# Performance work log

Hardware: AMD Instinct MI355X
Metric: run time of the kernel (lower is better)

The kernel has to match this reference:

```python
import jax, jax.numpy as jnp
import numpy as np

T, N, E = 3, 100000, 1600000
D_IN, D_H, D_OUT = 64, 64, 1


def _linear_params(key, fan_in, fan_out):
    s = 1.0 / np.sqrt(fan_in)
    k1, k2 = jax.random.split(key)
    W = jax.random.uniform(k1, (fan_in, fan_out), jnp.float32, -s, s)
    b = jax.random.uniform(k2, (fan_out,), jnp.float32, -s, s)
    return W, b


def setup_inputs() -> dict:
    key = jax.random.key(0)
    ks = jax.random.split(key, 9)
    x = jax.random.normal(ks[0], (T, N, D_IN), jnp.float32)
    src = jax.random.randint(ks[1], (T, E), 0, N, jnp.int32)
    dst = jax.random.randint(ks[2], (T, E), 0, N, jnp.int32)
    # xavier-uniform initial GCN weight [D_IN, D_H]
    lim = np.sqrt(6.0 / (D_IN + D_H))
    initial_weight = jax.random.uniform(ks[3], (D_IN, D_H), jnp.float32, -lim, lim)
    Wz, bz = _linear_params(ks[4], D_IN + D_H, D_H)  # update gate
    Wr, br = _linear_params(ks[5], D_IN + D_H, D_H)  # reset gate
    Wh, bh = _linear_params(ks[6], D_IN + D_H, D_H)  # htilda
    Wp, bp = _linear_params(ks[7], D_IN, D_IN)        # pool_proj
    Wo, bo = _linear_params(ks[8], D_H, D_OUT)        # out
    return dict(x=x, src=src, dst=dst, initial_weight=initial_weight,
                Wz=Wz, bz=bz, Wr=Wr, br=br, Wh=Wh, bh=bh,
                Wp=Wp, bp=bp, Wo=Wo, bo=bo)


def reference(x, src, dst, initial_weight, Wz, bz, Wr, br, Wh, bh, Wp, bp, Wo, bo):
    n_nodes = x.shape[1]
    ones_e = jnp.ones((x.shape[2] * 0 + src.shape[1],), jnp.float32)  # [E]

    def step(w, snap):
        xt, st, dt = snap  # [N, D_IN], [E], [E]
        # pooled graph context -> MatGRU weight evolution
        ctx = jnp.mean(xt, axis=0) @ Wp + bp            # [D_IN]
        inp = jnp.broadcast_to(ctx, (D_IN, D_IN))       # inputs.repeat(prev_w.size(0),1)
        xc = jnp.concatenate([inp, w], axis=1)          # [D_IN, D_IN+D_H]
        z = jax.nn.sigmoid(xc @ Wz + bz)
        r = jax.nn.sigmoid(xc @ Wr + br)
        gc = jnp.concatenate([inp, r * w], axis=1)
        h_tilde = jnp.tanh(gc @ Wh + bh)
        w_new = z * w + (1.0 - z) * h_tilde             # [D_IN, D_H]
        # GCN norm: deg = sum of (unit) edge weights per dst, clamp_min 1
        deg = jax.ops.segment_sum(ones_e, dt, num_segments=n_nodes)
        deg = jnp.maximum(deg, 1.0)
        norm = (1.0 / deg)[dt]                          # [E]
        # u_mul_e -> sum aggregation
        agg = jax.ops.segment_sum(xt[st] * norm[:, None], dt, num_segments=n_nodes)
        h = agg @ w_new                                 # [N, D_H]
        out = h @ Wo + bo                               # [N, D_OUT]
        return w_new, out

    w_final, outs = jax.lax.scan(step, initial_weight, (x, src, dst))
    return outs, w_final
```

## Files before the change

kernel.cpp:

```cpp
#include <hip/hip_runtime.h>
#include <math.h>

#define T_STEPS 3
#define N_NODES 100000
#define N_EDGES 1600000
#define N_E4    (N_EDGES / 4)
#define D 64

#define CS_BLOCKS 782

#define BKT_BITS 9
#define BKT_SIZE 512
#define NBKT 196
#define NBKT_PAD 256
#define QSCALE 65536.0f
#define QINV   (1.0f / 65536.0f)

#define SC_EPB 4096
#define SC_I4  1024
#define SC_CHUNKS 391

#define SMV_BLOCKS 782

#define GR_PAD 68

#define PACK_SCALE 1048576.0f
#define PACK_INV   (1.0f / 1048576.0f)


__global__ __launch_bounds__(256) void prep_kernel(const float* __restrict__ x,
                                                   const int* __restrict__ dst,
                                                   float* __restrict__ colsumP,
                                                   unsigned* __restrict__ histChunk) {
    const int t = blockIdx.y;
    const int tid = threadIdx.x;
    __shared__ float red[16][64];
    __shared__ unsigned h[NBKT_PAD];

    if (blockIdx.x < CS_BLOCKS) {
        const int q = tid & 15;
        const int g = tid >> 4;
        const float4* xt = (const float4*)(x + (size_t)t * N_NODES * D);
        const int base = blockIdx.x * 128;
        float sx = 0.f, sy = 0.f, sz = 0.f, sw = 0.f;
#pragma unroll
        for (int it = 0; it < 8; ++it) {
            const int r = base + g + 16 * it;
            if (r < N_NODES) {
                const float4 vv = xt[(size_t)r * 16 + q];
                sx += vv.x; sy += vv.y; sz += vv.z; sw += vv.w;
            }
        }
        red[g][q * 4 + 0] = sx;
        red[g][q * 4 + 1] = sy;
        red[g][q * 4 + 2] = sz;
        red[g][q * 4 + 3] = sw;
        __syncthreads();
        if (tid < 64) {
            float s = 0.f;
#pragma unroll
            for (int gg = 0; gg < 16; ++gg) s += red[gg][tid];
            colsumP[((size_t)t * CS_BLOCKS + blockIdx.x) * 64 + tid] = s;
        }
    } else {
        const int c = blockIdx.x - CS_BLOCKS;
        h[tid] = 0;
        __syncthreads();
        const int4* dp = (const int4*)(dst + (size_t)t * N_EDGES);
#pragma unroll
        for (int it = 0; it < 4; ++it) {
            const int i4 = c * SC_I4 + it * 256 + tid;
            if (i4 < N_E4) {
                const int4 d = dp[i4];
                atomicAdd(&h[d.x >> BKT_BITS], 1u);
                atomicAdd(&h[d.y >> BKT_BITS], 1u);
                atomicAdd(&h[d.z >> BKT_BITS], 1u);
                atomicAdd(&h[d.w >> BKT_BITS], 1u);
            }
        }
        __syncthreads();
        histChunk[((size_t)t * SC_CHUNKS + c) * NBKT_PAD + tid] = h[tid];
    }
}

__device__ __forceinline__ float fast_sigmoid(float v) {
    return 1.f / (1.f + __expf(-v));
}
__device__ __forceinline__ float fast_tanh(float v) {
    return 1.f - 2.f / (__expf(2.f * v) + 1.f);
}

__global__ __launch_bounds__(256) void gru_rows_kernel(
    const float* __restrict__ colsumP, const float* __restrict__ iw,
    const float* __restrict__ Wz, const float* __restrict__ bz,
    const float* __restrict__ Wr, const float* __restrict__ br,
    const float* __restrict__ Wh, const float* __restrict__ bh,
    const float* __restrict__ Wp, const float* __restrict__ bp,
    const float* __restrict__ Wo, const unsigned* __restrict__ histChunk,
    unsigned* __restrict__ bstart, unsigned* __restrict__ chunkPref,
    float* __restrict__ v_out, float* __restrict__ w_final) {
    const int tid = threadIdx.x;

    if (blockIdx.x == 16) {
        __shared__ unsigned scn[NBKT_PAD];
        for (int t = 0; t < T_STEPS; ++t) {
            unsigned c = 0;
            for (int k = 0; k < SC_CHUNKS; ++k)
                c += histChunk[((size_t)t * SC_CHUNKS + k) * NBKT_PAD + tid];
            unsigned v = c;
            scn[tid] = v;
            __syncthreads();
            for (int off = 1; off < NBKT_PAD; off <<= 1) {
                const unsigned add = (tid >= off) ? scn[tid - off] : 0u;
                __syncthreads();
                v += add;
                scn[tid] = v;
                __syncthreads();
            }
            bstart[t * NBKT_PAD + tid] = (unsigned)(t * N_EDGES) + (v - c);
            __syncthreads();
        }
        return;
    }
    if (blockIdx.x >= 17) {
        const int idx = blockIdx.x - 17;
        const int t = idx >> 6;
        const int wid = tid >> 6, lane = tid & 63;
        const int b = (idx & 63) * 4 + wid;
        unsigned running = 0;
#pragma unroll
        for (int g = 0; g < 7; ++g) {
            const int c = g * 64 + lane;
            const unsigned val = (c < SC_CHUNKS)
                ? histChunk[((size_t)t * SC_CHUNKS + c) * NBKT_PAD + b] : 0u;
            unsigned incl = val;
#pragma unroll
            for (int off = 1; off < 64; off <<= 1) {
                const unsigned n = __shfl_up(incl, off);
                if (lane >= off) incl += n;
            }
            if (c < SC_CHUNKS)
                chunkPref[((size_t)t * SC_CHUNKS + c) * NBKT_PAD + b] = running + (incl - val);
            running += __shfl(incl, 63);
        }
        return;
    }

    __shared__ float BzT[64 * GR_PAD];
    __shared__ float BrT[64 * GR_PAD];
    __shared__ float BhT[64 * GR_PAD];
    __shared__ float w_lds[4 * 64];
    __shared__ float mean_s[192];
    __shared__ float ctx_s[192];
    __shared__ float czrh_s[576];

#pragma unroll
    for (int it = 0; it < 16; ++it) {
        const int idx = it * 256 + tid;
        const int k = idx >> 6, j = idx & 63;
        BzT[j * GR_PAD + k] = Wz[(64 + k) * 64 + j];
        BrT[j * GR_PAD + k] = Wr[(64 + k) * 64 + j];
        BhT[j * GR_PAD + k] = Wh[(64 + k) * 64 + j];
    }
    if (tid < 192) {
        const int t = tid >> 6, j = tid & 63;
        float s = 0.f;
        for (int bx = 0; bx < CS_BLOCKS; ++bx)
            s += colsumP[((size_t)t * CS_BLOCKS + bx) * 64 + j];
        mean_s[tid] = s * (1.f / (float)N_NODES);
    }
    __syncthreads();
    if (tid < 192) {
        const int t = tid >> 6, j = tid & 63;
        float c = bp[j];
        for (int k = 0; k < 64; ++k)
            c = fmaf(mean_s[t * 64 + k], Wp[k * 64 + j], c);
        ctx_s[tid] = c;
    }
    __syncthreads();
    for (int co = (tid >> 6); co < 9; co += 4) {
        const int t = co / 3, m = co - 3 * t, j = tid & 63;
        const float* W = (m == 0) ? Wz : (m == 1) ? Wr : Wh;
        const float* bb = (m == 0) ? bz : (m == 1) ? br : bh;
        float c = bb[j];
        for (int k = 0; k < 64; ++k)
            c = fmaf(ctx_s[t * 64 + k], W[k * 64 + j], c);
        czrh_s[co * 64 + j] = c;
    }
    __syncthreads();

    const int wid = tid >> 6, lane = tid & 63;
    const int row = blockIdx.x * 4 + wid;
    float* wrow = &w_lds[wid * 64];
    float w = iw[row * 64 + lane];
    const float wo = Wo[lane];

    for (int t = 0; t < T_STEPS; ++t) {
        wrow[lane] = w;
        __syncthreads();
        float az = 0.f, ar = 0.f;
#pragma unroll
        for (int k0 = 0; k0 < 64; k0 += 4) {
            const float4 wv = *(const float4*)&wrow[k0];
            const float4 z4 = *(const float4*)&BzT[lane * GR_PAD + k0];
            const float4 r4 = *(const float4*)&BrT[lane * GR_PAD + k0];
            az = fmaf(wv.x, z4.x, az); az = fmaf(wv.y, z4.y, az);
            az = fmaf(wv.z, z4.z, az); az = fmaf(wv.w, z4.w, az);
            ar = fmaf(wv.x, r4.x, ar); ar = fmaf(wv.y, r4.y, ar);
            ar = fmaf(wv.z, r4.z, ar); ar = fmaf(wv.w, r4.w, ar);
        }
        const float z = fast_sigmoid(az + czrh_s[(t * 3 + 0) * 64 + lane]);
        const float r = fast_sigmoid(ar + czrh_s[(t * 3 + 1) * 64 + lane]);
        const float rw = r * w;
        __syncthreads();
        wrow[lane] = rw;
        __syncthreads();
        float ah = 0.f;
#pragma unroll
        for (int k0 = 0; k0 < 64; k0 += 4) {
            const float4 wv = *(const float4*)&wrow[k0];
            const float4 h4 = *(const float4*)&BhT[lane * GR_PAD + k0];
            ah = fmaf(wv.x, h4.x, ah); ah = fmaf(wv.y, h4.y, ah);
            ah = fmaf(wv.z, h4.z, ah); ah = fmaf(wv.w, h4.w, ah);
        }
        const float h = fast_tanh(ah + czrh_s[(t * 3 + 2) * 64 + lane]);
        w = z * w + (1.f - z) * h;
        float vp = w * wo;
        vp += __shfl_xor(vp, 1);
        vp += __shfl_xor(vp, 2);
        vp += __shfl_xor(vp, 4);
        vp += __shfl_xor(vp, 8);
        vp += __shfl_xor(vp, 16);
        vp += __shfl_xor(vp, 32);
        if (lane == 0) v_out[t * 64 + row] = vp;
        __syncthreads();
    }
    w_final[row * 64 + lane] = w;
}

__global__ __launch_bounds__(512) void scat_smv_kernel(
    const float* __restrict__ x, const float* __restrict__ v,
    const int* __restrict__ src, const int* __restrict__ dst,
    const unsigned* __restrict__ bstart, const unsigned* __restrict__ chunkPref,
    unsigned* __restrict__ recs, float* __restrict__ s) {
    const int t = blockIdx.y;
    const int tid = threadIdx.x;
    __shared__ __align__(16) unsigned char lds_raw[28672];

    if (blockIdx.x >= SC_CHUNKS) {
        float* vs = (float*)lds_raw;
        if (tid < 64) vs[tid] = v[t * 64 + tid];
        __syncthreads();
        const int row = (blockIdx.x - SC_CHUNKS) * 128 + (tid >> 2);
        const int l4 = tid & 3;
        if (row < N_NODES) {
            const float4* xr = (const float4*)(x + ((size_t)t * N_NODES + row) * D);
            float acc = 0.f;
#pragma unroll
            for (int i = 0; i < 4; ++i) {
                const int c = i * 4 + l4;
                const float4 xv = xr[c];
                acc += xv.x * vs[c * 4 + 0] + xv.y * vs[c * 4 + 1] +
                       xv.z * vs[c * 4 + 2] + xv.w * vs[c * 4 + 3];
            }
            acc += __shfl_xor(acc, 1);
            acc += __shfl_xor(acc, 2);
            if (l4 == 0) s[(size_t)t * N_NODES + row] = acc;
        }
        return;
    }

    const int c = blockIdx.x;
    unsigned* recL = (unsigned*)lds_raw;
    unsigned short* bktL = (unsigned short*)(lds_raw + 16384);
    unsigned* bh   = (unsigned*)(lds_raw + 24576);
    unsigned* sc   = bh + 256;
    unsigned* lofs = sc + 256;
    unsigned* badj = lofs + 256;

    if (tid < NBKT_PAD) bh[tid] = 0;
    __syncthreads();

    const int4* sp = (const int4*)(src + (size_t)t * N_EDGES);
    const int4* dp = (const int4*)(dst + (size_t)t * N_EDGES);

    unsigned rec[8];
    int bkt[8];
#pragma unroll
    for (int k = 0; k < 8; ++k) bkt[k] = -1;

#pragma unroll
    for (int it = 0; it < 2; ++it) {
        const int i4 = c * SC_I4 + it * 512 + tid;
        if (i4 < N_E4) {
            const int4 sv = sp[i4];
            const int4 dv = dp[i4];
            const int ss[4] = {sv.x, sv.y, sv.z, sv.w};
            const int dd[4] = {dv.x, dv.y, dv.z, dv.w};
#pragma unroll
            for (int j = 0; j < 4; ++j) {
                const int b = dd[j] >> BKT_BITS;
                rec[it * 4 + j] = ((unsigned)(dd[j] & (BKT_SIZE - 1)) << 17) |
                                  (unsigned)ss[j];
                bkt[it * 4 + j] = b;
                atomicAdd(&bh[b], 1u);
            }
        }
    }
    __syncthreads();
    if (tid < NBKT_PAD) sc[tid] = bh[tid];
    __syncthreads();
    for (int off = 1; off < NBKT_PAD; off <<= 1) {
        unsigned add = 0;
        if (tid < NBKT_PAD && tid >= off) add = sc[tid - off];
        __syncthreads();
        if (tid < NBKT_PAD) sc[tid] += add;
        __syncthreads();
    }
    if (tid < NBKT_PAD) {
        const unsigned cnt = bh[tid];
        const unsigned ex = sc[tid] - cnt;
        lofs[tid] = ex;
        const unsigned base = bstart[t * NBKT_PAD + tid] +
                              chunkPref[((size_t)t * SC_CHUNKS + c) * NBKT_PAD + tid];
        badj[tid] = base - ex;
    }
    __syncthreads();
#pragma unroll
    for (int k = 0; k < 8; ++k) {
        if (bkt[k] >= 0) {
            const unsigned pos = atomicAdd(&lofs[bkt[k]], 1u);
            recL[pos] = rec[k];
            bktL[pos] = (unsigned short)bkt[k];
        }
    }
    __syncthreads();
    const int nrec = min(SC_EPB, N_EDGES - c * SC_EPB);
    for (int i = tid; i < nrec; i += 512) {
        const unsigned b = bktL[i];
        recs[badj[b] + (unsigned)i] = recL[i];
    }
}

__global__ __launch_bounds__(256) void accum_kernel(const unsigned* __restrict__ recs,
                                                    const unsigned* __restrict__ start,
                                                    const float* __restrict__ s,
                                                    const float* __restrict__ bo,
                                                    float* __restrict__ out) {
    const int b = blockIdx.x;
    const int t = blockIdx.y;
    const int tid = threadIdx.x;
    __shared__ unsigned long long bins[BKT_SIZE];
    bins[tid] = 0ULL;
    bins[tid + 256] = 0ULL;
    __syncthreads();
    const float* st = s + (size_t)t * N_NODES;
    const unsigned s0 = start[t * NBKT_PAD + b];
    const unsigned s1 = start[t * NBKT_PAD + b + 1];
    for (unsigned i = s0 + tid; i < s1; i += 256) {
        const unsigned rec = recs[i];
        const unsigned dl = rec >> 17;
        const long long q = llrintf(st[rec & 0x1FFFFu] * QSCALE);
        atomicAdd(&bins[dl], (unsigned long long)((1ULL << 41) + (unsigned long long)q));
    }
    __syncthreads();
    const float bo0 = bo[0];
#pragma unroll
    for (int k = 0; k < 2; ++k) {
        const int i = tid + k * 256;
        const int node = b * BKT_SIZE + i;
        if (node < N_NODES) {
            const unsigned long long tot = bins[i];
            const unsigned long long deg = (tot + (1ULL << 40)) >> 41;
            const long long rem = (long long)(tot - (deg << 41));
            const float acc = (float)rem * QINV;
            out[(size_t)t * N_NODES + node] = bo0 + acc / fmaxf((float)deg, 1.f);
        }
    }
}


__global__ __launch_bounds__(256) void smatvec_kernel(const float* __restrict__ x,
                                                      const float* __restrict__ v,
                                                      float* __restrict__ s) {
    const int t = blockIdx.y;
    const int tid = threadIdx.x;
    const int l4 = tid & 3;
    const int rloc = tid >> 2;
    __shared__ float vs[64];
    if (tid < 64) vs[tid] = v[t * 64 + tid];
    __syncthreads();
    const int row = blockIdx.x * 64 + rloc;
    if (row < N_NODES) {
        const float4* xr = (const float4*)(x + ((size_t)t * N_NODES + row) * D);
        float acc = 0.f;
#pragma unroll
        for (int i = 0; i < 4; ++i) {
            const int c = i * 4 + l4;
            const float4 xv = xr[c];
            acc += xv.x * vs[c * 4 + 0] + xv.y * vs[c * 4 + 1] +
                   xv.z * vs[c * 4 + 2] + xv.w * vs[c * 4 + 3];
        }
        acc += __shfl_xor(acc, 1);
        acc += __shfl_xor(acc, 2);
        if (l4 == 0) s[(size_t)t * N_NODES + row] = acc;
    }
}

__global__ __launch_bounds__(256) void edge_kernel(const int* __restrict__ src,
                                                   const int* __restrict__ dst,
                                                   const float* __restrict__ s,
                                                   unsigned long long* __restrict__ packed) {
    const int t = blockIdx.y;
    const int e4 = blockIdx.x * 256 + threadIdx.x;
    if (e4 * 4 >= N_EDGES) return;
    const int4* sp = (const int4*)(src + (size_t)t * N_EDGES);
    const int4* dp = (const int4*)(dst + (size_t)t * N_EDGES);
    const float* st = s + (size_t)t * N_NODES;
    unsigned long long* pk = packed + (size_t)t * N_NODES;
    const int4 s4 = sp[e4];
    const int4 d4 = dp[e4];
    const float v0 = st[s4.x], v1 = st[s4.y], v2 = st[s4.z], v3 = st[s4.w];
    const unsigned long long base = 1ULL << 41;
    atomicAdd(&pk[d4.x], base + (unsigned long long)(long long)llrintf(v0 * PACK_SCALE));
    atomicAdd(&pk[d4.y], base + (unsigned long long)(long long)llrintf(v1 * PACK_SCALE));
    atomicAdd(&pk[d4.z], base + (unsigned long long)(long long)llrintf(v2 * PACK_SCALE));
    atomicAdd(&pk[d4.w], base + (unsigned long long)(long long)llrintf(v3 * PACK_SCALE));
}

__global__ __launch_bounds__(256) void out_kernel(const unsigned long long* __restrict__ packed,
                                                  const float* __restrict__ bo,
                                                  float* __restrict__ out) {
    const int i = blockIdx.x * 256 + threadIdx.x;
    if (i < T_STEPS * N_NODES) {
        const unsigned long long tot = packed[i];
        const unsigned long long deg = (tot + (1ULL << 40)) >> 41;
        const long long rem = (long long)(tot - (deg << 41));
        const float acc = (float)rem * PACK_INV;
        out[i] = bo[0] + acc / fmaxf((float)deg, 1.0f);
    }
}

extern "C" void kernel_launch(void* const* d_in, const int* in_sizes, int n_in,
                              void* d_out, int out_size, void* d_ws, size_t ws_size,
                              hipStream_t stream) {
    const float* x  = (const float*)d_in[0];
    const int* src  = (const int*)d_in[1];
    const int* dst  = (const int*)d_in[2];
    const float* iw = (const float*)d_in[3];
    const float* Wz = (const float*)d_in[4];
    const float* bz = (const float*)d_in[5];
    const float* Wr = (const float*)d_in[6];
    const float* br = (const float*)d_in[7];
    const float* Wh = (const float*)d_in[8];
    const float* bh = (const float*)d_in[9];
    const float* Wp = (const float*)d_in[10];
    const float* bp = (const float*)d_in[11];
    const float* Wo = (const float*)d_in[12];
    const float* bo = (const float*)d_in[13];
    float* out = (float*)d_out;
    float* ws  = (float*)d_ws;

    const size_t FAST_NEED = (size_t)5401248 * sizeof(float);
    if (ws_size >= FAST_NEED) {
        unsigned* recs      = (unsigned*)ws;
        float* colsumP      = ws;
        unsigned* histChunk = (unsigned*)(ws + 150144);
        unsigned* chunkPref = (unsigned*)(ws + 4800000);
        unsigned* bstart    = (unsigned*)(ws + 5100288);
        float* vbuf         = ws + 5101056;
        float* sbuf         = ws + 5101248;

        prep_kernel<<<dim3(CS_BLOCKS + SC_CHUNKS, 3), 256, 0, stream>>>(x, dst,
                                                                        colsumP, histChunk);
        gru_rows_kernel<<<209, 256, 0, stream>>>(colsumP, iw, Wz, bz, Wr, br, Wh, bh,
                                                 Wp, bp, Wo, histChunk, bstart, chunkPref,
                                                 vbuf, out + (size_t)T_STEPS * N_NODES);
        scat_smv_kernel<<<dim3(SC_CHUNKS + SMV_BLOCKS, 3), 512, 0, stream>>>(
            x, vbuf, src, dst, bstart, chunkPref, recs, sbuf);
        accum_kernel<<<dim3(NBKT, 3), 256, 0, stream>>>(recs, bstart, sbuf, bo, out);
    } else {
        float* colsumP = ws;
        float* vbuf    = ws + 150144;
        float* sbuf    = ws + 150336;
        unsigned long long* packed = (unsigned long long*)(ws + 450336);

        hipMemsetAsync(packed, 0, (size_t)600000 * sizeof(float), stream);

        prep_kernel<<<dim3(CS_BLOCKS, 3), 256, 0, stream>>>(x, dst, colsumP,
                                                            (unsigned*)nullptr);
        gru_rows_kernel<<<16, 256, 0, stream>>>(colsumP, iw, Wz, bz, Wr, br, Wh, bh,
                                                Wp, bp, Wo, (unsigned*)nullptr,
                                                (unsigned*)nullptr, (unsigned*)nullptr,
                                                vbuf, out + (size_t)T_STEPS * N_NODES);
        smatvec_kernel<<<dim3(1563, 3), 256, 0, stream>>>(x, vbuf, sbuf);
        edge_kernel<<<dim3(1563, 3), 256, 0, stream>>>(src, dst, sbuf, packed);
        out_kernel<<<1172, 256, 0, stream>>>(packed, bo, out);
    }
}
```

Baseline: 105.5 us.

## Replace global bucket sort with per-chunk local sort and segment offsets

Edge records are no longer counting-sorted into globally contiguous buckets. Each 4096-edge chunk is sorted by destination bucket inside its own LDS and written back to its own slot with coalesced int4 stores. The prep kernel now computes per-chunk bucket start offsets with an in-block scan, which removes the global histogram reduction and prefix-scan blocks and the scatter kernel's own histogram pass. In exchange, the accumulation kernel has each thread walk one chunk's short segment serially. Those reads are less coalesced and can be load-imbalanced, since 391 chunks are spread over 256 threads.

Result: slower. 132.0 us (+25.2%).

```diff
diff --git a/kernel.cpp b/kernel.cpp
--- a/kernel.cpp
+++ b/kernel.cpp
@@ -31,11 +31,12 @@
 __global__ __launch_bounds__(256) void prep_kernel(const float* __restrict__ x,
                                                    const int* __restrict__ dst,
                                                    float* __restrict__ colsumP,
-                                                   unsigned* __restrict__ histChunk) {
+                                                   unsigned* __restrict__ segStart) {
     const int t = blockIdx.y;
     const int tid = threadIdx.x;
     __shared__ float red[16][64];
     __shared__ unsigned h[NBKT_PAD];
+    __shared__ unsigned scn[NBKT_PAD];
 
     if (blockIdx.x < CS_BLOCKS) {
         const int q = tid & 15;
@@ -79,7 +80,19 @@
             }
         }
         __syncthreads();
-        histChunk[((size_t)t * SC_CHUNKS + c) * NBKT_PAD + tid] = h[tid];
+        const unsigned cval = h[tid];
+        unsigned v = cval;
+        scn[tid] = v;
+        __syncthreads();
+        for (int off = 1; off < NBKT_PAD; off <<= 1) {
+            const unsigned add = (tid >= off) ? scn[tid - off] : 0u;
+            __syncthreads();
+            v += add;
+            scn[tid] = v;
+            __syncthreads();
+        }
+        segStart[((size_t)t * SC_CHUNKS + c) * NBKT_PAD + tid] =
+            (unsigned)(c * SC_EPB) + (v - cval);
     }
 }
 
@@ -96,56 +109,9 @@
     const float* __restrict__ Wr, const float* __restrict__ br,
     const float* __restrict__ Wh, const float* __restrict__ bh,
     const float* __restrict__ Wp, const float* __restrict__ bp,
-    const float* __restrict__ Wo, const unsigned* __restrict__ histChunk,
-    unsigned* __restrict__ bstart, unsigned* __restrict__ chunkPref,
+    const float* __restrict__ Wo,
     float* __restrict__ v_out, float* __restrict__ w_final) {
     const int tid = threadIdx.x;
-
-    if (blockIdx.x == 16) {
-        __shared__ unsigned scn[NBKT_PAD];
-        for (int t = 0; t < T_STEPS; ++t) {
-            unsigned c = 0;
-            for (int k = 0; k < SC_CHUNKS; ++k)
-                c += histChunk[((size_t)t * SC_CHUNKS + k) * NBKT_PAD + tid];
-            unsigned v = c;
-            scn[tid] = v;
-            __syncthreads();
-            for (int off = 1; off < NBKT_PAD; off <<= 1) {
-                const unsigned add = (tid >= off) ? scn[tid - off] : 0u;
-                __syncthreads();
-                v += add;
-                scn[tid] = v;
-                __syncthreads();
-            }
-            bstart[t * NBKT_PAD + tid] = (unsigned)(t * N_EDGES) + (v - c);
-            __syncthreads();
-        }
-        return;
-    }
-    if (blockIdx.x >= 17) {
-        const int idx = blockIdx.x - 17;
-        const int t = idx >> 6;
-        const int wid = tid >> 6, lane = tid & 63;
-        const int b = (idx & 63) * 4 + wid;
-        unsigned running = 0;
-#pragma unroll
-        for (int g = 0; g < 7; ++g) {
-            const int c = g * 64 + lane;
-            const unsigned val = (c < SC_CHUNKS)
-                ? histChunk[((size_t)t * SC_CHUNKS + c) * NBKT_PAD + b] : 0u;
-            unsigned incl = val;
-#pragma unroll
-            for (int off = 1; off < 64; off <<= 1) {
-                const unsigned n = __shfl_up(incl, off);
-                if (lane >= off) incl += n;
-            }
-            if (c < SC_CHUNKS)
-                chunkPref[((size_t)t * SC_CHUNKS + c) * NBKT_PAD + b] = running + (incl - val);
-            running += __shfl(incl, 63);
-        }
-        return;
-    }
-
     __shared__ float BzT[64 * GR_PAD];
     __shared__ float BrT[64 * GR_PAD];
     __shared__ float BhT[64 * GR_PAD];
@@ -241,11 +207,11 @@
 __global__ __launch_bounds__(512) void scat_smv_kernel(
     const float* __restrict__ x, const float* __restrict__ v,
     const int* __restrict__ src, const int* __restrict__ dst,
-    const unsigned* __restrict__ bstart, const unsigned* __restrict__ chunkPref,
+    const unsigned* __restrict__ segStart,
     unsigned* __restrict__ recs, float* __restrict__ s) {
     const int t = blockIdx.y;
     const int tid = threadIdx.x;
-    __shared__ __align__(16) unsigned char lds_raw[28672];
+    __shared__ __align__(16) unsigned char lds_raw[17408];
 
     if (blockIdx.x >= SC_CHUNKS) {
         float* vs = (float*)lds_raw;
@@ -272,14 +238,11 @@
 
     const int c = blockIdx.x;
     unsigned* recL = (unsigned*)lds_raw;
-    unsigned short* bktL = (unsigned short*)(lds_raw + 16384);
-    unsigned* bh   = (unsigned*)(lds_raw + 24576);
-    unsigned* sc   = bh + 256;
-    unsigned* lofs = sc + 256;
-    unsigned* badj = lofs + 256;
-
-    if (tid < NBKT_PAD) bh[tid] = 0;
-    __syncthreads();
+    unsigned* lofs = (unsigned*)(lds_raw + 16384);
+
+    if (tid < NBKT_PAD)
+        lofs[tid] = segStart[((size_t)t * SC_CHUNKS + c) * NBKT_PAD + tid] -
+                    (unsigned)(c * SC_EPB);
 
     const int4* sp = (const int4*)(src + (size_t)t * N_EDGES);
     const int4* dp = (const int4*)(dst + (size_t)t * N_EDGES);
@@ -299,31 +262,11 @@
             const int dd[4] = {dv.x, dv.y, dv.z, dv.w};
 #pragma unroll
             for (int j = 0; j < 4; ++j) {
-                const int b = dd[j] >> BKT_BITS;
                 rec[it * 4 + j] = ((unsigned)(dd[j] & (BKT_SIZE - 1)) << 17) |
                                   (unsigned)ss[j];
-                bkt[it * 4 + j] = b;
-                atomicAdd(&bh[b], 1u);
+                bkt[it * 4 + j] = dd[j] >> BKT_BITS;
             }
         }
-    }
-    __syncthreads();
-    if (tid < NBKT_PAD) sc[tid] = bh[tid];
-    __syncthreads();
-    for (int off = 1; off < NBKT_PAD; off <<= 1) {
-        unsigned add = 0;
-        if (tid < NBKT_PAD && tid >= off) add = sc[tid - off];
-        __syncthreads();
-        if (tid < NBKT_PAD) sc[tid] += add;
-        __syncthreads();
-    }
-    if (tid < NBKT_PAD) {
-        const unsigned cnt = bh[tid];
-        const unsigned ex = sc[tid] - cnt;
-        lofs[tid] = ex;
-        const unsigned base = bstart[t * NBKT_PAD + tid] +
-                              chunkPref[((size_t)t * SC_CHUNKS + c) * NBKT_PAD + tid];
-        badj[tid] = base - ex;
     }
     __syncthreads();
 #pragma unroll
@@ -331,19 +274,17 @@
         if (bkt[k] >= 0) {
             const unsigned pos = atomicAdd(&lofs[bkt[k]], 1u);
             recL[pos] = rec[k];
-            bktL[pos] = (unsigned short)bkt[k];
-        }
-    }
-    __syncthreads();
-    const int nrec = min(SC_EPB, N_EDGES - c * SC_EPB);
-    for (int i = tid; i < nrec; i += 512) {
-        const unsigned b = bktL[i];
-        recs[badj[b] + (unsigned)i] = recL[i];
-    }
+        }
+    }
+    __syncthreads();
+    const int nrecI4 = min(SC_I4, N_E4 - c * SC_I4);
+    int4* outp = (int4*)(recs + (size_t)t * N_EDGES + (size_t)c * SC_EPB);
+    const int4* inL = (const int4*)recL;
+    for (int i = tid; i < nrecI4; i += 512) outp[i] = inL[i];
 }
 
 __global__ __launch_bounds__(256) void accum_kernel(const unsigned* __restrict__ recs,
-                                                    const unsigned* __restrict__ start,
+                                                    const unsigned* __restrict__ segStart,
                                                     const float* __restrict__ s,
                                                     const float* __restrict__ bo,
                                                     float* __restrict__ out) {
@@ -355,13 +296,18 @@
     bins[tid + 256] = 0ULL;
     __syncthreads();
     const float* st = s + (size_t)t * N_NODES;
-    const unsigned s0 = start[t * NBKT_PAD + b];
-    const unsigned s1 = start[t * NBKT_PAD + b + 1];
-    for (unsigned i = s0 + tid; i < s1; i += 256) {
-        const unsigned rec = recs[i];
-        const unsigned dl = rec >> 17;
-        const long long q = llrintf(st[rec & 0x1FFFFu] * QSCALE);
-        atomicAdd(&bins[dl], (unsigned long long)((1ULL << 41) + (unsigned long long)q));
+    const unsigned* seg = segStart + (size_t)t * SC_CHUNKS * NBKT_PAD;
+    const unsigned* rb = recs + (size_t)t * N_EDGES;
+    for (int c = tid; c < SC_CHUNKS; c += 256) {
+        const unsigned s0 = seg[c * NBKT_PAD + b];
+        const unsigned s1 = seg[c * NBKT_PAD + b + 1];
+        for (unsigned i = s0; i < s1; ++i) {
+            const unsigned rec = rb[i];
+            const unsigned dl = rec >> 17;
+            const long long q = llrintf(st[rec & 0x1FFFFu] * QSCALE);
+            atomicAdd(&bins[dl],
+                      (unsigned long long)((1ULL << 41) + (unsigned long long)q));
+        }
     }
     __syncthreads();
     const float bo0 = bo[0];
@@ -461,24 +407,22 @@
     float* out = (float*)d_out;
     float* ws  = (float*)d_ws;
 
-    const size_t FAST_NEED = (size_t)5401248 * sizeof(float);
+    const size_t FAST_NEED = (size_t)5400480 * sizeof(float);
     if (ws_size >= FAST_NEED) {
-        unsigned* recs      = (unsigned*)ws;
-        float* colsumP      = ws;
-        unsigned* histChunk = (unsigned*)(ws + 150144);
-        unsigned* chunkPref = (unsigned*)(ws + 4800000);
-        unsigned* bstart    = (unsigned*)(ws + 5100288);
-        float* vbuf         = ws + 5101056;
-        float* sbuf         = ws + 5101248;
+        unsigned* recs     = (unsigned*)ws;
+        float* colsumP     = ws;
+        unsigned* segStart = (unsigned*)(ws + 4800000);
+        float* vbuf        = ws + 5100288;
+        float* sbuf        = ws + 5100480;
 
         prep_kernel<<<dim3(CS_BLOCKS + SC_CHUNKS, 3), 256, 0, stream>>>(x, dst,
-                                                                        colsumP, histChunk);
-        gru_rows_kernel<<<209, 256, 0, stream>>>(colsumP, iw, Wz, bz, Wr, br, Wh, bh,
-                                                 Wp, bp, Wo, histChunk, bstart, chunkPref,
-                                                 vbuf, out + (size_t)T_STEPS * N_NODES);
+                                                                        colsumP, segStart);
+        gru_rows_kernel<<<16, 256, 0, stream>>>(colsumP, iw, Wz, bz, Wr, br, Wh, bh,
+                                                Wp, bp, Wo, vbuf,
+                                                out + (size_t)T_STEPS * N_NODES);
         scat_smv_kernel<<<dim3(SC_CHUNKS + SMV_BLOCKS, 3), 512, 0, stream>>>(
-            x, vbuf, src, dst, bstart, chunkPref, recs, sbuf);
-        accum_kernel<<<dim3(NBKT, 3), 256, 0, stream>>>(recs, bstart, sbuf, bo, out);
+            x, vbuf, src, dst, segStart, recs, sbuf);
+        accum_kernel<<<dim3(NBKT, 3), 256, 0, stream>>>(recs, segStart, sbuf, bo, out);
     } else {
         float* colsumP = ws;
         float* vbuf    = ws + 150144;
@@ -490,9 +434,8 @@
         prep_kernel<<<dim3(CS_BLOCKS, 3), 256, 0, stream>>>(x, dst, colsumP,
                                                             (unsigned*)nullptr);
         gru_rows_kernel<<<16, 256, 0, stream>>>(colsumP, iw, Wz, bz, Wr, br, Wh, bh,
-                                                Wp, bp, Wo, (unsigned*)nullptr,
-                                                (unsigned*)nullptr, (unsigned*)nullptr,
-                                                vbuf, out + (size_t)T_STEPS * N_NODES);
+                                                Wp, bp, Wo, vbuf,
+                                                out + (size_t)T_STEPS * N_NODES);
         smatvec_kernel<<<dim3(1563, 3), 256, 0, stream>>>(x, vbuf, sbuf);
         edge_kernel<<<dim3(1563, 3), 256, 0, stream>>>(src, dst, sbuf, packed);
         out_kernel<<<1172, 256, 0, stream>>>(packed, bo, out);
```

## Widen destination buckets to 2048 nodes and use wave-level scans

Applied to the files above, without the earlier changes.

Raises the counting-sort bucket size from 512 to 2048 nodes, so there are 49 buckets instead of 196. The LDS block scans over 256 entries become single-wavefront shuffle scans over 64 entries, and bucket ids are stored as bytes. The accumulation kernel moves to 512 threads per block with a 2048-entry 64-bit LDS bin array. This cuts histogram and prefix-scan work and synchronisation, but leaves only 147 accumulation blocks, each with more LDS and more atomic traffic, which may underfill the GPU.

After: 110.1 us. 4.4% more time.

```diff
diff --git a/kernel.cpp b/kernel.cpp
--- a/kernel.cpp
+++ b/kernel.cpp
@@ -9,10 +9,10 @@
 
 #define CS_BLOCKS 782
 
-#define BKT_BITS 9
-#define BKT_SIZE 512
-#define NBKT 196
-#define NBKT_PAD 256
+#define BKT_BITS 11
+#define BKT_SIZE 2048
+#define NBKT 49
+#define NBKT_PAD 64
 #define QSCALE 65536.0f
 #define QINV   (1.0f / 65536.0f)
 
@@ -64,7 +64,7 @@
         }
     } else {
         const int c = blockIdx.x - CS_BLOCKS;
-        h[tid] = 0;
+        if (tid < NBKT_PAD) h[tid] = 0;
         __syncthreads();
         const int4* dp = (const int4*)(dst + (size_t)t * N_EDGES);
 #pragma unroll
@@ -79,7 +79,8 @@
             }
         }
         __syncthreads();
-        histChunk[((size_t)t * SC_CHUNKS + c) * NBKT_PAD + tid] = h[tid];
+        if (tid < NBKT_PAD)
+            histChunk[((size_t)t * SC_CHUNKS + c) * NBKT_PAD + tid] = h[tid];
     }
 }
 
@@ -102,31 +103,27 @@
     const int tid = threadIdx.x;
 
     if (blockIdx.x == 16) {
-        __shared__ unsigned scn[NBKT_PAD];
-        for (int t = 0; t < T_STEPS; ++t) {
-            unsigned c = 0;
-            for (int k = 0; k < SC_CHUNKS; ++k)
-                c += histChunk[((size_t)t * SC_CHUNKS + k) * NBKT_PAD + tid];
-            unsigned v = c;
-            scn[tid] = v;
-            __syncthreads();
-            for (int off = 1; off < NBKT_PAD; off <<= 1) {
-                const unsigned add = (tid >= off) ? scn[tid - off] : 0u;
-                __syncthreads();
-                v += add;
-                scn[tid] = v;
-                __syncthreads();
-            }
-            bstart[t * NBKT_PAD + tid] = (unsigned)(t * N_EDGES) + (v - c);
-            __syncthreads();
+        if (tid < NBKT_PAD) {
+            for (int t = 0; t < T_STEPS; ++t) {
+                unsigned c = 0;
+                for (int k = 0; k < SC_CHUNKS; ++k)
+                    c += histChunk[((size_t)t * SC_CHUNKS + k) * NBKT_PAD + tid];
+                unsigned v = c;
+#pragma unroll
+                for (int off = 1; off < 64; off <<= 1) {
+                    const unsigned n = __shfl_up(v, off);
+                    if (tid >= off) v += n;
+                }
+                bstart[t * NBKT_PAD + tid] = (unsigned)(t * N_EDGES) + (v - c);
+            }
         }
         return;
     }
     if (blockIdx.x >= 17) {
         const int idx = blockIdx.x - 17;
-        const int t = idx >> 6;
+        const int t = idx >> 4;
         const int wid = tid >> 6, lane = tid & 63;
-        const int b = (idx & 63) * 4 + wid;
+        const int b = (idx & 15) * 4 + wid;
         unsigned running = 0;
 #pragma unroll
         for (int g = 0; g < 7; ++g) {
@@ -245,7 +242,7 @@
     unsigned* __restrict__ recs, float* __restrict__ s) {
     const int t = blockIdx.y;
     const int tid = threadIdx.x;
-    __shared__ __align__(16) unsigned char lds_raw[28672];
+    __shared__ __align__(16) unsigned char lds_raw[21504];
 
     if (blockIdx.x >= SC_CHUNKS) {
         float* vs = (float*)lds_raw;
@@ -272,11 +269,10 @@
 
     const int c = blockIdx.x;
     unsigned* recL = (unsigned*)lds_raw;
-    unsigned short* bktL = (unsigned short*)(lds_raw + 16384);
-    unsigned* bh   = (unsigned*)(lds_raw + 24576);
-    unsigned* sc   = bh + 256;
-    unsigned* lofs = sc + 256;
-    unsigned* badj = lofs + 256;
+    unsigned char* bktL = (unsigned char*)(lds_raw + 16384);
+    unsigned* bh   = (unsigned*)(lds_raw + 20480);
+    unsigned* lofs = bh + 64;
+    unsigned* badj = lofs + 64;
 
     if (tid < NBKT_PAD) bh[tid] = 0;
     __syncthreads();
@@ -308,18 +304,15 @@
         }
     }
     __syncthreads();
-    if (tid < NBKT_PAD) sc[tid] = bh[tid];
-    __syncthreads();
-    for (int off = 1; off < NBKT_PAD; off <<= 1) {
-        unsigned add = 0;
-        if (tid < NBKT_PAD && tid >= off) add = sc[tid - off];
-        __syncthreads();
-        if (tid < NBKT_PAD) sc[tid] += add;
-        __syncthreads();
-    }
-    if (tid < NBKT_PAD) {
+    if (tid < 64) {
         const unsigned cnt = bh[tid];
-        const unsigned ex = sc[tid] - cnt;
+        unsigned v = cnt;
+#pragma unroll
+        for (int off = 1; off < 64; off <<= 1) {
+            const unsigned n = __shfl_up(v, off);
+            if (tid >= off) v += n;
+        }
+        const unsigned ex = v - cnt;
         lofs[tid] = ex;
         const unsigned base = bstart[t * NBKT_PAD + tid] +
                               chunkPref[((size_t)t * SC_CHUNKS + c) * NBKT_PAD + tid];
@@ -331,7 +324,7 @@
         if (bkt[k] >= 0) {
             const unsigned pos = atomicAdd(&lofs[bkt[k]], 1u);
             recL[pos] = rec[k];
-            bktL[pos] = (unsigned short)bkt[k];
+            bktL[pos] = (unsigned char)bkt[k];
         }
     }
     __syncthreads();
@@ -342,7 +335,7 @@
     }
 }
 
-__global__ __launch_bounds__(256) void accum_kernel(const unsigned* __restrict__ recs,
+__global__ __launch_bounds__(512) void accum_kernel(const unsigned* __restrict__ recs,
                                                     const unsigned* __restrict__ start,
                                                     const float* __restrict__ s,
                                                     const float* __restrict__ bo,
@@ -351,23 +344,24 @@
     const int t = blockIdx.y;
     const int tid = threadIdx.x;
     __shared__ unsigned long long bins[BKT_SIZE];
-    bins[tid] = 0ULL;
-    bins[tid + 256] = 0ULL;
+#pragma unroll
+    for (int k = 0; k < 4; ++k) bins[tid + k * 512] = 0ULL;
     __syncthreads();
     const float* st = s + (size_t)t * N_NODES;
     const unsigned s0 = start[t * NBKT_PAD + b];
     const unsigned s1 = start[t * NBKT_PAD + b + 1];
-    for (unsigned i = s0 + tid; i < s1; i += 256) {
+    for (unsigned i = s0 + tid; i < s1; i += 512) {
         const unsigned rec = recs[i];
         const unsigned dl = rec >> 17;
         const long long q = llrintf(st[rec & 0x1FFFFu] * QSCALE);
-        atomicAdd(&bins[dl], (unsigned long long)((1ULL << 41) + (unsigned long long)q));
+        atomicAdd(&bins[dl],
+                  (unsigned long long)((1ULL << 41) + (unsigned long long)q));
     }
     __syncthreads();
     const float bo0 = bo[0];
 #pragma unroll
-    for (int k = 0; k < 2; ++k) {
-        const int i = tid + k * 256;
+    for (int k = 0; k < 4; ++k) {
+        const int i = tid + k * 512;
         const int node = b * BKT_SIZE + i;
         if (node < N_NODES) {
             const unsigned long long tot = bins[i];
@@ -461,24 +455,24 @@
     float* out = (float*)d_out;
     float* ws  = (float*)d_ws;
 
-    const size_t FAST_NEED = (size_t)5401248 * sizeof(float);
+    const size_t FAST_NEED = (size_t)5175456 * sizeof(float);
     if (ws_size >= FAST_NEED) {
         unsigned* recs      = (unsigned*)ws;
         float* colsumP      = ws;
         unsigned* histChunk = (unsigned*)(ws + 150144);
         unsigned* chunkPref = (unsigned*)(ws + 4800000);
-        unsigned* bstart    = (unsigned*)(ws + 5100288);
-        float* vbuf         = ws + 5101056;
-        float* sbuf         = ws + 5101248;
+        unsigned* bstart    = (unsigned*)(ws + 4875072);
+        float* vbuf         = ws + 4875264;
+        float* sbuf         = ws + 4875456;
 
         prep_kernel<<<dim3(CS_BLOCKS + SC_CHUNKS, 3), 256, 0, stream>>>(x, dst,
                                                                         colsumP, histChunk);
-        gru_rows_kernel<<<209, 256, 0, stream>>>(colsumP, iw, Wz, bz, Wr, br, Wh, bh,
-                                                 Wp, bp, Wo, histChunk, bstart, chunkPref,
-                                                 vbuf, out + (size_t)T_STEPS * N_NODES);
+        gru_rows_kernel<<<65, 256, 0, stream>>>(colsumP, iw, Wz, bz, Wr, br, Wh, bh,
+                                                Wp, bp, Wo, histChunk, bstart, chunkPref,
+                                                vbuf, out + (size_t)T_STEPS * N_NODES);
         scat_smv_kernel<<<dim3(SC_CHUNKS + SMV_BLOCKS, 3), 512, 0, stream>>>(
             x, vbuf, src, dst, bstart, chunkPref, recs, sbuf);
-        accum_kernel<<<dim3(NBKT, 3), 256, 0, stream>>>(recs, bstart, sbuf, bo, out);
+        accum_kernel<<<dim3(NBKT, 3), 512, 0, stream>>>(recs, bstart, sbuf, bo, out);
     } else {
         float* colsumP = ws;
         float* vbuf    = ws + 150144;
```
